# Kernel optimization log

Hardware: AMD Instinct MI355X
Metric: run time of the kernel (lower is better)

## Reference

```python
import jax, jax.numpy as jnp
import numpy as np

EMBED_DIM = 768
NUM_HEADS = 12
HEAD_DIM = EMBED_DIM // NUM_HEADS


def setup_inputs() -> dict:
    key = jax.random.key(0)
    ks = jax.random.split(key, 9)
    B, N, D = 8, 1024, EMBED_DIM
    s = 1.0 / np.sqrt(D)
    x = jax.random.normal(ks[0], (B, N, D), dtype=jnp.float32)
    Wq = jax.random.normal(ks[1], (D, D), dtype=jnp.float32) * s
    bq = jnp.zeros((D,), dtype=jnp.float32)
    Wk = jax.random.normal(ks[2], (D, D), dtype=jnp.float32) * s
    bk = jnp.zeros((D,), dtype=jnp.float32)
    Wv = jax.random.normal(ks[3], (D, D), dtype=jnp.float32) * s
    bv = jnp.zeros((D,), dtype=jnp.float32)
    Wo = jax.random.normal(ks[4], (D, D), dtype=jnp.float32) * s
    bo = jnp.zeros((D,), dtype=jnp.float32)
    return {"x": x, "Wq": Wq, "bq": bq, "Wk": Wk, "bk": bk,
            "Wv": Wv, "bv": bv, "Wo": Wo, "bo": bo}


def reference(x, Wq, bq, Wk, bk, Wv, bv, Wo, bo):
    B, N, D = x.shape
    H, Hd = NUM_HEADS, HEAD_DIM
    # torch Linear: y = x @ W.T + b
    q = (x @ Wq.T + bq).reshape(B, N, H, Hd).transpose(0, 2, 1, 3)  # [B,H,N,Hd]
    k = (x @ Wk.T + bk).reshape(B, N, H, Hd).transpose(0, 2, 1, 3)
    v = (x @ Wv.T + bv).reshape(B, N, H, Hd).transpose(0, 2, 1, 3)
    # NOTE: original scales by embed_dim**-0.5 (not head_dim)
    scale = jnp.asarray(D, x.dtype) ** -0.5
    scores = jnp.einsum('bhnd,bhmd->bhnm', q, k) * scale  # [B,H,N,N]
    attn = jax.nn.softmax(scores, axis=-1)
    out = jnp.einsum('bhnm,bhmd->bhnd', attn, v)  # dropout: identity in eval
    out = out.transpose(0, 2, 1, 3).reshape(B, N, D)
    return out @ Wo.T + bo
```

## Files before the change

kernel.cpp:

```cpp
#include <hip/hip_runtime.h>
#include <math.h>


typedef __bf16 bf16x8 __attribute__((ext_vector_type(8)));
typedef float  f32x4  __attribute__((ext_vector_type(4)));
typedef unsigned u32x2 __attribute__((ext_vector_type(2)));
typedef unsigned u32x4 __attribute__((ext_vector_type(4)));
typedef unsigned short ushort_t;

__device__ __forceinline__ unsigned short f2bf(float f) {
    unsigned u = __float_as_uint(f);
    u += 0x7fffu + ((u >> 16) & 1u);
    return (unsigned short)(u >> 16);
}

#define GLL16(g, l)                                                                        \
    __builtin_amdgcn_global_load_lds((const __attribute__((address_space(1))) void*)(g),   \
                                     (__attribute__((address_space(3))) void*)(l), 16, 0, 0)

__global__ __launch_bounds__(256)
void cast_all(const float* __restrict__ x,
              const float* __restrict__ w0, const float* __restrict__ w1,
              const float* __restrict__ w2, const float* __restrict__ w3,
              ushort_t* __restrict__ xb, ushort_t* __restrict__ wb0,
              ushort_t* __restrict__ wb1, ushort_t* __restrict__ wb2,
              ushort_t* __restrict__ wb3)
{
    const int y = blockIdx.y;
    const float* s; ushort_t* d; int n;
    switch (y) {
        case 0:  s = x;  d = xb;  n = 8192 * 768; break;
        case 1:  s = w0; d = wb0; n = 768 * 768;  break;
        case 2:  s = w1; d = wb1; n = 768 * 768;  break;
        case 3:  s = w2; d = wb2; n = 768 * 768;  break;
        default: s = w3; d = wb3; n = 768 * 768;  break;
    }
    const int i = (blockIdx.x * 256 + threadIdx.x) * 8;
    if (i >= n) return;
    const float4 f0 = *(const float4*)(s + i);
    const float4 f1 = *(const float4*)(s + i + 4);
    ushort4 p0, p1;
    p0.x = f2bf(f0.x); p0.y = f2bf(f0.y); p0.z = f2bf(f0.z); p0.w = f2bf(f0.w);
    p1.x = f2bf(f1.x); p1.y = f2bf(f1.y); p1.z = f2bf(f1.z); p1.w = f2bf(f1.w);
    *(ushort4*)(d + i)     = p0;
    *(ushort4*)(d + i + 4) = p1;
}

__device__ __forceinline__ void gemm_core_mfma(
    const ushort_t* __restrict__ A, const ushort_t* __restrict__ W,
    int m0, int n0, f32x4 acc[4][4])
{
    __shared__ ushort_t As[128 * 32];
    __shared__ ushort_t Ws[128 * 32];
    const int tid = threadIdx.x;
    const int L   = tid & 63;
    const int wv  = tid >> 6;
    const int wr  = wv >> 1, wc = wv & 1;
    const int c   = L & 15,  g  = L >> 4;

    const int c0 = tid, c1 = tid + 256;
    const ushort_t* a0 = A + (size_t)(m0 + (c0 >> 2)) * 768 + (c0 & 3) * 8;
    const ushort_t* a1 = A + (size_t)(m0 + (c1 >> 2)) * 768 + (c1 & 3) * 8;
    const ushort_t* w0 = W + (size_t)(n0 + (c0 >> 2)) * 768 + (c0 & 3) * 8;
    const ushort_t* w1 = W + (size_t)(n0 + (c1 >> 2)) * 768 + (c1 & 3) * 8;

#pragma unroll
    for (int i = 0; i < 4; ++i)
#pragma unroll
        for (int j = 0; j < 4; ++j) acc[i][j] = (f32x4){0.f, 0.f, 0.f, 0.f};

    for (int k0 = 0; k0 < 768; k0 += 32) {
        __syncthreads();
        GLL16(a0 + k0, &As[(size_t)c0 * 8]);
        GLL16(a1 + k0, &As[(size_t)c1 * 8]);
        GLL16(w0 + k0, &Ws[(size_t)c0 * 8]);
        GLL16(w1 + k0, &Ws[(size_t)c1 * 8]);
        __syncthreads();
        bf16x8 af[4], bfr[4];
#pragma unroll
        for (int i = 0; i < 4; ++i)
            af[i] = *(const bf16x8*)&As[(wr * 64 + i * 16 + c) * 32 + g * 8];
#pragma unroll
        for (int j = 0; j < 4; ++j)
            bfr[j] = *(const bf16x8*)&Ws[(wc * 64 + j * 16 + c) * 32 + g * 8];
#pragma unroll
        for (int i = 0; i < 4; ++i)
#pragma unroll
            for (int j = 0; j < 4; ++j)
                acc[i][j] = __builtin_amdgcn_mfma_f32_16x16x32_bf16(
                    af[i], bfr[j], acc[i][j], 0, 0, 0);
    }
}

__global__ __launch_bounds__(256, 2)
void gemm_qkv(const ushort_t* __restrict__ xb,
              const ushort_t* __restrict__ wqb, const ushort_t* __restrict__ wkb,
              const ushort_t* __restrict__ wvb,
              const float* __restrict__ bq, const float* __restrict__ bk,
              const float* __restrict__ bv,
              ushort_t* __restrict__ Qh, ushort_t* __restrict__ Kl,
              ushort_t* __restrict__ Vl)
{
    const int z = blockIdx.z;
    const ushort_t* W   = (z == 0) ? wqb : (z == 1) ? wkb : wvb;
    const float*    bia = (z == 0) ? bq  : (z == 1) ? bk  : bv;
    const int m0 = blockIdx.y * 128, n0 = blockIdx.x * 128;
    f32x4 acc[4][4];
    gemm_core_mfma(xb, W, m0, n0, acc);

    const int tid = threadIdx.x, L = tid & 63, wv2 = tid >> 6;
    const int wr = wv2 >> 1, wc = wv2 & 1, c = L & 15, g = L >> 4;
#pragma unroll
    for (int i = 0; i < 4; ++i) {
        const int row0 = m0 + wr * 64 + i * 16 + g * 4;
        const int b = row0 >> 10;
        const int n = row0 & 1023;
#pragma unroll
        for (int j = 0; j < 4; ++j) {
            const int col = n0 + wc * 64 + j * 16 + c;
            const int h = col >> 6, hd = col & 63;
            const int bh = b * 12 + h;
            const float bsv = bia[col];
            if (z == 0) {
                ushort_t* dst = Qh + ((size_t)bh * 1024 + n) * 64 + hd;
#pragma unroll
                for (int r = 0; r < 4; ++r)
                    dst[(size_t)r * 64] = f2bf(acc[i][j][r] + bsv);
            } else if (z == 1) {
                const int tau = n >> 4, cK = n & 15;
                const int u = hd >> 5, gK = (hd >> 3) & 3, j8 = hd & 7;
                ushort_t* dst = Kl + (((size_t)bh * 64 + tau) * 2 + u) * 512
                              + gK * 128 + cK * 8 + j8;
#pragma unroll
                for (int r = 0; r < 4; ++r)
                    dst[r * 8] = f2bf(acc[i][j][r] + bsv);
            } else {
                const int ht = hd >> 4, cV = hd & 15;
                const int T = n >> 6, u = (n >> 5) & 1, gV = (n >> 3) & 3, j0 = n & 7;
                ushort4 pk;
                pk.x = f2bf(acc[i][j][0] + bsv);
                pk.y = f2bf(acc[i][j][1] + bsv);
                pk.z = f2bf(acc[i][j][2] + bsv);
                pk.w = f2bf(acc[i][j][3] + bsv);
                *(ushort4*)&Vl[(((size_t)(bh * 4 + ht) * 16 + T) * 2 + u) * 512
                               + gV * 128 + cV * 8 + j0] = pk;
            }
        }
    }
}

__global__ __launch_bounds__(256, 2)
void gemm_outp(const ushort_t* __restrict__ attnb, const ushort_t* __restrict__ wob,
               const float* __restrict__ bo, float* __restrict__ out)
{
    const int m0 = blockIdx.y * 128, n0 = blockIdx.x * 128;
    f32x4 acc[4][4];
    gemm_core_mfma(attnb, wob, m0, n0, acc);
    const int tid = threadIdx.x, L = tid & 63, wv2 = tid >> 6;
    const int wr = wv2 >> 1, wc = wv2 & 1, c = L & 15, g = L >> 4;
#pragma unroll
    for (int i = 0; i < 4; ++i) {
        const int row = m0 + wr * 64 + i * 16 + g * 4;
#pragma unroll
        for (int j = 0; j < 4; ++j) {
            const int col = n0 + wc * 64 + j * 16 + c;
            const float bsv = bo[col];
#pragma unroll
            for (int r = 0; r < 4; ++r)
                out[(size_t)(row + r) * 768 + col] = acc[i][j][r] + bsv;
        }
    }
}

__global__ __launch_bounds__(64, 3)
void flash_bf16(const ushort_t* __restrict__ Q, const ushort_t* __restrict__ Kl,
                const ushort_t* __restrict__ Vl, ushort_t* __restrict__ attnb)
{
    __shared__ ushort_t Ps[2][16 * 68];
    const int L = threadIdx.x;
    const int c = L & 15, g = L >> 4;
    const int bh = blockIdx.y, q0 = blockIdx.x * 32;
    const float SC2 = 0.05205954985329743f;

    const ushort_t* Qp = Q + ((size_t)bh * 1024 + q0 + c) * 64 + g * 8;
    bf16x8 qf[2][2];
    qf[0][0] = *(const bf16x8*)Qp;
    qf[0][1] = *(const bf16x8*)(Qp + 32);
    qf[1][0] = *(const bf16x8*)(Qp + 16 * 64);
    qf[1][1] = *(const bf16x8*)(Qp + 16 * 64 + 32);

    const ushort_t* Kb = Kl + (size_t)bh * 65536 + (size_t)L * 8;
    const ushort_t* Vb = Vl + (size_t)bh * 65536 + (size_t)L * 8;

    f32x4 o[2][4];
#pragma unroll
    for (int w = 0; w < 2; ++w)
#pragma unroll
        for (int ht = 0; ht < 4; ++ht) o[w][ht] = (f32x4){0.f, 0.f, 0.f, 0.f};
    float ls[2] = {0.f, 0.f};

    bf16x8 kf0[4], kf1[4];
#pragma unroll
    for (int ct = 0; ct < 4; ++ct) {
        kf0[ct] = *(const bf16x8*)(Kb + (size_t)(ct * 2 + 0) * 512);
        kf1[ct] = *(const bf16x8*)(Kb + (size_t)(ct * 2 + 1) * 512);
    }

    for (int T = 0; T < 16; ++T) {
        bf16x8 vf0[4], vf1[4];
#pragma unroll
        for (int ht = 0; ht < 4; ++ht) {
            const ushort_t* vp = Vb + (size_t)((ht * 16 + T) * 2) * 512;
            vf0[ht] = *(const bf16x8*)vp;
            vf1[ht] = *(const bf16x8*)(vp + 512);
        }
        f32x4 s[2][4];
#pragma unroll
        for (int w = 0; w < 2; ++w)
#pragma unroll
            for (int ct = 0; ct < 4; ++ct) {
                f32x4 zz = (f32x4){0.f, 0.f, 0.f, 0.f};
                zz = __builtin_amdgcn_mfma_f32_16x16x32_bf16(kf0[ct], qf[w][0], zz, 0, 0, 0);
                zz = __builtin_amdgcn_mfma_f32_16x16x32_bf16(kf1[ct], qf[w][1], zz, 0, 0, 0);
                s[w][ct] = zz;
            }
        const int Tn = (T < 15) ? T + 1 : 15;
#pragma unroll
        for (int ct = 0; ct < 4; ++ct) {
            const ushort_t* kp = Kb + (size_t)((Tn * 4 + ct) * 2) * 512;
            kf0[ct] = *(const bf16x8*)kp;
            kf1[ct] = *(const bf16x8*)(kp + 512);
        }
#pragma unroll
        for (int w = 0; w < 2; ++w) {
            unsigned pw[4][2];
#pragma unroll
            for (int ct = 0; ct < 4; ++ct) {
                float p[4];
#pragma unroll
                for (int r = 0; r < 4; ++r) p[r] = exp2f(s[w][ct][r] * SC2);
                const unsigned w01 = __builtin_amdgcn_perm(
                    __float_as_uint(p[1]), __float_as_uint(p[0]), 0x07060302u);
                const unsigned w23 = __builtin_amdgcn_perm(
                    __float_as_uint(p[3]), __float_as_uint(p[2]), 0x07060302u);
                pw[ct][0] = w01;
                pw[ct][1] = w23;
                ls[w] += __uint_as_float(w01 << 16) + __uint_as_float(w01 & 0xffff0000u)
                       + __uint_as_float(w23 << 16) + __uint_as_float(w23 & 0xffff0000u);
            }
#pragma unroll
            for (int ct = 0; ct < 4; ++ct)
                *(u32x2*)&Ps[w][c * 68 + ct * 16 + g * 4] = (u32x2){pw[ct][0], pw[ct][1]};
        }
#pragma unroll
        for (int w = 0; w < 2; ++w) {
            const int pb = c * 68 + g * 8;
            const u32x4 pa  = *(const u32x4*)&Ps[w][pb];
            const u32x4 pbv = *(const u32x4*)&Ps[w][pb + 32];
            const bf16x8 pf0 = __builtin_bit_cast(bf16x8, pa);
            const bf16x8 pf1 = __builtin_bit_cast(bf16x8, pbv);
#pragma unroll
            for (int ht = 0; ht < 4; ++ht) {
                o[w][ht] = __builtin_amdgcn_mfma_f32_16x16x32_bf16(vf0[ht], pf0, o[w][ht], 0, 0, 0);
                o[w][ht] = __builtin_amdgcn_mfma_f32_16x16x32_bf16(vf1[ht], pf1, o[w][ht], 0, 0, 0);
            }
        }
    }

    const int b = bh / 12, h = bh % 12;
#pragma unroll
    for (int w = 0; w < 2; ++w) {
        float l = ls[w];
        l += __shfl_xor(l, 16);
        l += __shfl_xor(l, 32);
        const float inv = 1.f / l;
#pragma unroll
        for (int ht = 0; ht < 4; ++ht) {
            const unsigned w0 = (unsigned)f2bf(o[w][ht][0] * inv)
                              | ((unsigned)f2bf(o[w][ht][1] * inv) << 16);
            const unsigned w1 = (unsigned)f2bf(o[w][ht][2] * inv)
                              | ((unsigned)f2bf(o[w][ht][3] * inv) << 16);
            *(u32x2*)&Ps[w][c * 68 + ht * 16 + g * 4] = (u32x2){w0, w1};
        }
#pragma unroll
        for (int e = 0; e < 2; ++e) {
            const int row = e * 8 + (L >> 3);
            const int ch  = L & 7;
            const int si  = row * 68 + ch * 8;
            const u32x2 t0 = *(const u32x2*)&Ps[w][si];
            const u32x2 t1 = *(const u32x2*)&Ps[w][si + 4];
            *(u32x4*)&attnb[((size_t)(b * 1024 + q0 + w * 16 + row)) * 768 + h * 64 + ch * 8]
                = (u32x4){t0.x, t0.y, t1.x, t1.y};
        }
    }
}

extern "C" void kernel_launch(void* const* d_in, const int* in_sizes, int n_in,
                              void* d_out, int out_size, void* d_ws, size_t ws_size,
                              hipStream_t stream)
{
    const float* x  = (const float*)d_in[0];
    const float* Wq = (const float*)d_in[1];
    const float* bq = (const float*)d_in[2];
    const float* Wk = (const float*)d_in[3];
    const float* bk = (const float*)d_in[4];
    const float* Wv = (const float*)d_in[5];
    const float* bv = (const float*)d_in[6];
    const float* Wo = (const float*)d_in[7];
    const float* bo = (const float*)d_in[8];
    float* out = (float*)d_out;

    char* ws = (char*)d_ws;
    ushort_t* xb    = (ushort_t*)(ws);
    ushort_t* wqb   = (ushort_t*)(ws + 12582912);
    ushort_t* wkb   = (ushort_t*)(ws + 12582912 + 1179648);
    ushort_t* wvb   = (ushort_t*)(ws + 12582912 + 2359296);
    ushort_t* wob   = (ushort_t*)(ws + 12582912 + 3538944);
    ushort_t* Qh    = (ushort_t*)(ws + 17301504);
    ushort_t* Kl    = (ushort_t*)(ws + 29884416);
    ushort_t* Vl    = (ushort_t*)(ws + 42467328);
    ushort_t* attnb = (ushort_t*)(ws + 55050240);

    cast_all<<<dim3(3072, 5), 256, 0, stream>>>(x, Wq, Wk, Wv, Wo,
                                                xb, wqb, wkb, wvb, wob);
    gemm_qkv<<<dim3(6, 64, 3), 256, 0, stream>>>(xb, wqb, wkb, wvb,
                                                 bq, bk, bv, Qh, Kl, Vl);
    flash_bf16<<<dim3(32, 96), 64, 0, stream>>>(Qh, Kl, Vl, attnb);
    gemm_outp<<<dim3(6, 64), 256, 0, stream>>>(attnb, wob, bo, out);
}
```

Baseline: 212.9 us.

## Split flash KV loop across two waves and stage QKV epilogue stores through LDS

The flash attention kernel now runs two waves per block, each covering half of the key/value tiles. Their partial outputs and row sums are merged through shared memory, which is valid because the softmax uses no running max. The QKV GEMM epilogue now stages each 16-row tile in shared memory so Q, K and V are written with 16-byte vector stores instead of scattered 2-byte stores. This adds an LDS merge and barrier in exchange for more parallelism per query tile, and it drops the previous K prefetch pipelining.

```diff
diff --git a/kernel.cpp b/kernel.cpp
--- a/kernel.cpp
+++ b/kernel.cpp
@@ -12,6 +12,9 @@
     unsigned u = __float_as_uint(f);
     u += 0x7fffu + ((u >> 16) & 1u);
     return (unsigned short)(u >> 16);
+}
+__device__ __forceinline__ unsigned pk16(unsigned short lo, unsigned short hi) {
+    return (unsigned)lo | ((unsigned)hi << 16);
 }
 
 #define GLL16(g, l)                                                                        \
@@ -48,10 +51,10 @@
 
 __device__ __forceinline__ void gemm_core_mfma(
     const ushort_t* __restrict__ A, const ushort_t* __restrict__ W,
-    int m0, int n0, f32x4 acc[4][4])
-{
-    __shared__ ushort_t As[128 * 32];
-    __shared__ ushort_t Ws[128 * 32];
+    int m0, int n0, ushort_t* smem, f32x4 acc[4][4])
+{
+    ushort_t* As = smem;
+    ushort_t* Ws = smem + 4096;
     const int tid = threadIdx.x;
     const int L   = tid & 63;
     const int wv  = tid >> 6;
@@ -101,50 +104,70 @@
               ushort_t* __restrict__ Qh, ushort_t* __restrict__ Kl,
               ushort_t* __restrict__ Vl)
 {
+    __shared__ ushort_t smem[8192];
     const int z = blockIdx.z;
     const ushort_t* W   = (z == 0) ? wqb : (z == 1) ? wkb : wvb;
     const float*    bia = (z == 0) ? bq  : (z == 1) ? bk  : bv;
     const int m0 = blockIdx.y * 128, n0 = blockIdx.x * 128;
     f32x4 acc[4][4];
-    gemm_core_mfma(xb, W, m0, n0, acc);
+    gemm_core_mfma(xb, W, m0, n0, smem, acc);
 
     const int tid = threadIdx.x, L = tid & 63, wv2 = tid >> 6;
     const int wr = wv2 >> 1, wc = wv2 & 1, c = L & 15, g = L >> 4;
+    ushort_t* scr = smem + wv2 * 1280;
+    const int h = (n0 + wc * 64) >> 6;
+    float bsv[4];
+#pragma unroll
+    for (int j = 0; j < 4; ++j) bsv[j] = bia[n0 + wc * 64 + j * 16 + c];
+
+    __syncthreads();
 #pragma unroll
     for (int i = 0; i < 4; ++i) {
-        const int row0 = m0 + wr * 64 + i * 16 + g * 4;
-        const int b = row0 >> 10;
-        const int n = row0 & 1023;
-#pragma unroll
-        for (int j = 0; j < 4; ++j) {
-            const int col = n0 + wc * 64 + j * 16 + c;
-            const int h = col >> 6, hd = col & 63;
-            const int bh = b * 12 + h;
-            const float bsv = bia[col];
+        const int rowg = m0 + wr * 64 + i * 16;
+        const int b  = rowg >> 10;
+        const int nb = rowg & 1023;
+        const int bh = b * 12 + h;
+        if (z < 2) {
+#pragma unroll
+            for (int j = 0; j < 4; ++j)
+#pragma unroll
+                for (int r = 0; r < 4; ++r)
+                    scr[(g * 4 + r) * 72 + j * 16 + c] = f2bf(acc[i][j][r] + bsv[j]);
             if (z == 0) {
-                ushort_t* dst = Qh + ((size_t)bh * 1024 + n) * 64 + hd;
-#pragma unroll
-                for (int r = 0; r < 4; ++r)
-                    dst[(size_t)r * 64] = f2bf(acc[i][j][r] + bsv);
-            } else if (z == 1) {
-                const int tau = n >> 4, cK = n & 15;
-                const int u = hd >> 5, gK = (hd >> 3) & 3, j8 = hd & 7;
-                ushort_t* dst = Kl + (((size_t)bh * 64 + tau) * 2 + u) * 512
-                              + gK * 128 + cK * 8 + j8;
-#pragma unroll
-                for (int r = 0; r < 4; ++r)
-                    dst[r * 8] = f2bf(acc[i][j][r] + bsv);
+                const int row = L >> 2, qp = L & 3;
+                const u32x4 v0 = *(const u32x4*)&scr[row * 72 + qp * 16];
+                const u32x4 v1 = *(const u32x4*)&scr[row * 72 + qp * 16 + 8];
+                ushort_t* dst = Qh + ((size_t)bh * 1024 + nb + row) * 64 + qp * 16;
+                *(u32x4*)dst       = v0;
+                *(u32x4*)(dst + 8) = v1;
             } else {
-                const int ht = hd >> 4, cV = hd & 15;
-                const int T = n >> 6, u = (n >> 5) & 1, gV = (n >> 3) & 3, j0 = n & 7;
-                ushort4 pk;
-                pk.x = f2bf(acc[i][j][0] + bsv);
-                pk.y = f2bf(acc[i][j][1] + bsv);
-                pk.z = f2bf(acc[i][j][2] + bsv);
-                pk.w = f2bf(acc[i][j][3] + bsv);
-                *(ushort4*)&Vl[(((size_t)(bh * 4 + ht) * 16 + T) * 2 + u) * 512
-                               + gV * 128 + cV * 8 + j0] = pk;
-            }
+                const int n16 = L >> 2, q1 = L & 3;
+                const u32x4 va = *(const u32x4*)&scr[n16 * 72 + q1 * 8];
+                const u32x4 vb2 = *(const u32x4*)&scr[n16 * 72 + q1 * 8 + 32];
+                ushort_t* base = Kl + (size_t)bh * 65536 + (size_t)(nb >> 4) * 1024;
+                *(u32x4*)&base[q1 * 128 + n16 * 8]       = va;
+                *(u32x4*)&base[512 + q1 * 128 + n16 * 8] = vb2;
+            }
+        } else {
+#pragma unroll
+            for (int j = 0; j < 4; ++j) {
+                const unsigned w01 = pk16(f2bf(acc[i][j][0] + bsv[j]),
+                                          f2bf(acc[i][j][1] + bsv[j]));
+                const unsigned w23 = pk16(f2bf(acc[i][j][2] + bsv[j]),
+                                          f2bf(acc[i][j][3] + bsv[j]));
+                const int a = (j * 16 + c) * 20 + g * 4;
+                *(unsigned*)&scr[a]     = w01;
+                *(unsigned*)&scr[a + 2] = w23;
+            }
+            const u32x2 r0 = *(const u32x2*)&scr[L * 20];
+            const u32x2 r1 = *(const u32x2*)&scr[L * 20 + 4];
+            const u32x2 r2 = *(const u32x2*)&scr[L * 20 + 8];
+            const u32x2 r3 = *(const u32x2*)&scr[L * 20 + 12];
+            const int ht = L >> 4, cV = L & 15;
+            const int T = nb >> 6, u = (nb >> 5) & 1, gVa = (nb >> 3) & 3;
+            ushort_t* vb = Vl + (((size_t)(bh * 4 + ht) * 16 + T) * 2 + u) * 512 + cV * 8;
+            *(u32x4*)&vb[gVa * 128]       = (u32x4){r0.x, r0.y, r1.x, r1.y};
+            *(u32x4*)&vb[(gVa + 1) * 128] = (u32x4){r2.x, r2.y, r3.x, r3.y};
         }
     }
 }
@@ -153,9 +176,10 @@
 void gemm_outp(const ushort_t* __restrict__ attnb, const ushort_t* __restrict__ wob,
                const float* __restrict__ bo, float* __restrict__ out)
 {
+    __shared__ ushort_t smem[8192];
     const int m0 = blockIdx.y * 128, n0 = blockIdx.x * 128;
     f32x4 acc[4][4];
-    gemm_core_mfma(attnb, wob, m0, n0, acc);
+    gemm_core_mfma(attnb, wob, m0, n0, smem, acc);
     const int tid = threadIdx.x, L = tid & 63, wv2 = tid >> 6;
     const int wr = wv2 >> 1, wc = wv2 & 1, c = L & 15, g = L >> 4;
 #pragma unroll
@@ -164,21 +188,22 @@
 #pragma unroll
         for (int j = 0; j < 4; ++j) {
             const int col = n0 + wc * 64 + j * 16 + c;
-            const float bsv = bo[col];
+            const float bsvo = bo[col];
 #pragma unroll
             for (int r = 0; r < 4; ++r)
-                out[(size_t)(row + r) * 768 + col] = acc[i][j][r] + bsv;
-        }
-    }
-}
-
-__global__ __launch_bounds__(64, 3)
+                out[(size_t)(row + r) * 768 + col] = acc[i][j][r] + bsvo;
+        }
+    }
+}
+
+__global__ __launch_bounds__(128, 4)
 void flash_bf16(const ushort_t* __restrict__ Q, const ushort_t* __restrict__ Kl,
                 const ushort_t* __restrict__ Vl, ushort_t* __restrict__ attnb)
 {
-    __shared__ ushort_t Ps[2][16 * 68];
-    const int L = threadIdx.x;
-    const int c = L & 15, g = L >> 4;
+    __shared__ ushort_t Ps[2][2][16 * 68];
+    __shared__ f32x4 Comb[64 * 9];
+    const int tid = threadIdx.x;
+    const int wv = tid >> 6, L = tid & 63, c = L & 15, g = L >> 4;
     const int bh = blockIdx.y, q0 = blockIdx.x * 32;
     const float SC2 = 0.05205954985329743f;
 
@@ -186,8 +211,8 @@
     bf16x8 qf[2][2];
     qf[0][0] = *(const bf16x8*)Qp;
     qf[0][1] = *(const bf16x8*)(Qp + 32);
-    qf[1][0] = *(const bf16x8*)(Qp + 16 * 64);
-    qf[1][1] = *(const bf16x8*)(Qp + 16 * 64 + 32);
+    qf[1][0] = *(const bf16x8*)(Qp + 1024);
+    qf[1][1] = *(const bf16x8*)(Qp + 1056);
 
     const ushort_t* Kb = Kl + (size_t)bh * 65536 + (size_t)L * 8;
     const ushort_t* Vb = Vl + (size_t)bh * 65536 + (size_t)L * 8;
@@ -199,98 +224,99 @@
         for (int ht = 0; ht < 4; ++ht) o[w][ht] = (f32x4){0.f, 0.f, 0.f, 0.f};
     float ls[2] = {0.f, 0.f};
 
-    bf16x8 kf0[4], kf1[4];
-#pragma unroll
-    for (int ct = 0; ct < 4; ++ct) {
-        kf0[ct] = *(const bf16x8*)(Kb + (size_t)(ct * 2 + 0) * 512);
-        kf1[ct] = *(const bf16x8*)(Kb + (size_t)(ct * 2 + 1) * 512);
-    }
-
-    for (int T = 0; T < 16; ++T) {
-        bf16x8 vf0[4], vf1[4];
-#pragma unroll
-        for (int ht = 0; ht < 4; ++ht) {
-            const ushort_t* vp = Vb + (size_t)((ht * 16 + T) * 2) * 512;
-            vf0[ht] = *(const bf16x8*)vp;
-            vf1[ht] = *(const bf16x8*)(vp + 512);
-        }
-        f32x4 s[2][4];
-#pragma unroll
-        for (int w = 0; w < 2; ++w)
+    const int Tbeg = wv * 8;
+    for (int T = Tbeg; T < Tbeg + 8; ++T) {
+        bf16x8 kf0[4], kf1[4];
+#pragma unroll
+        for (int ct = 0; ct < 4; ++ct) {
+            const ushort_t* kp = Kb + (size_t)((T * 4 + ct) * 2) * 512;
+            kf0[ct] = *(const bf16x8*)kp;
+            kf1[ct] = *(const bf16x8*)(kp + 512);
+        }
+#pragma unroll
+        for (int w = 0; w < 2; ++w) {
+            f32x4 s[4];
 #pragma unroll
             for (int ct = 0; ct < 4; ++ct) {
                 f32x4 zz = (f32x4){0.f, 0.f, 0.f, 0.f};
                 zz = __builtin_amdgcn_mfma_f32_16x16x32_bf16(kf0[ct], qf[w][0], zz, 0, 0, 0);
                 zz = __builtin_amdgcn_mfma_f32_16x16x32_bf16(kf1[ct], qf[w][1], zz, 0, 0, 0);
-                s[w][ct] = zz;
-            }
-        const int Tn = (T < 15) ? T + 1 : 15;
-#pragma unroll
-        for (int ct = 0; ct < 4; ++ct) {
-            const ushort_t* kp = Kb + (size_t)((Tn * 4 + ct) * 2) * 512;
-            kf0[ct] = *(const bf16x8*)kp;
-            kf1[ct] = *(const bf16x8*)(kp + 512);
-        }
-#pragma unroll
-        for (int w = 0; w < 2; ++w) {
-            unsigned pw[4][2];
+                s[ct] = zz;
+            }
 #pragma unroll
             for (int ct = 0; ct < 4; ++ct) {
                 float p[4];
 #pragma unroll
-                for (int r = 0; r < 4; ++r) p[r] = exp2f(s[w][ct][r] * SC2);
+                for (int r = 0; r < 4; ++r) p[r] = exp2f(s[ct][r] * SC2);
                 const unsigned w01 = __builtin_amdgcn_perm(
                     __float_as_uint(p[1]), __float_as_uint(p[0]), 0x07060302u);
                 const unsigned w23 = __builtin_amdgcn_perm(
                     __float_as_uint(p[3]), __float_as_uint(p[2]), 0x07060302u);
-                pw[ct][0] = w01;
-                pw[ct][1] = w23;
                 ls[w] += __uint_as_float(w01 << 16) + __uint_as_float(w01 & 0xffff0000u)
                        + __uint_as_float(w23 << 16) + __uint_as_float(w23 & 0xffff0000u);
-            }
-#pragma unroll
-            for (int ct = 0; ct < 4; ++ct)
-                *(u32x2*)&Ps[w][c * 68 + ct * 16 + g * 4] = (u32x2){pw[ct][0], pw[ct][1]};
-        }
+                *(u32x2*)&Ps[wv][w][c * 68 + ct * 16 + g * 4] = (u32x2){w01, w23};
+            }
+        }
+        const int pb = c * 68 + g * 8;
+        bf16x8 pf[2][2];
 #pragma unroll
         for (int w = 0; w < 2; ++w) {
-            const int pb = c * 68 + g * 8;
-            const u32x4 pa  = *(const u32x4*)&Ps[w][pb];
-            const u32x4 pbv = *(const u32x4*)&Ps[w][pb + 32];
-            const bf16x8 pf0 = __builtin_bit_cast(bf16x8, pa);
-            const bf16x8 pf1 = __builtin_bit_cast(bf16x8, pbv);
+            pf[w][0] = __builtin_bit_cast(bf16x8, *(const u32x4*)&Ps[wv][w][pb]);
+            pf[w][1] = __builtin_bit_cast(bf16x8, *(const u32x4*)&Ps[wv][w][pb + 32]);
+        }
+#pragma unroll
+        for (int ht = 0; ht < 4; ++ht) {
+            const ushort_t* vp = Vb + (size_t)((ht * 16 + T) * 2) * 512;
+            const bf16x8 v0 = *(const bf16x8*)vp;
+            const bf16x8 v1 = *(const bf16x8*)(vp + 512);
+#pragma unroll
+            for (int w = 0; w < 2; ++w) {
+                o[w][ht] = __builtin_amdgcn_mfma_f32_16x16x32_bf16(v0, pf[w][0], o[w][ht], 0, 0, 0);
+                o[w][ht] = __builtin_amdgcn_mfma_f32_16x16x32_bf16(v1, pf[w][1], o[w][ht], 0, 0, 0);
+            }
+        }
+    }
+
+    if (wv == 1) {
+#pragma unroll
+        for (int w = 0; w < 2; ++w)
+#pragma unroll
+            for (int ht = 0; ht < 4; ++ht) Comb[L * 9 + w * 4 + ht] = o[w][ht];
+        Comb[L * 9 + 8] = (f32x4){ls[0], ls[1], 0.f, 0.f};
+    }
+    __syncthreads();
+    if (wv == 0) {
+#pragma unroll
+        for (int w = 0; w < 2; ++w)
+#pragma unroll
+            for (int ht = 0; ht < 4; ++ht) o[w][ht] += Comb[L * 9 + w * 4 + ht];
+        const f32x4 lw = Comb[L * 9 + 8];
+        ls[0] += lw.x;
+        ls[1] += lw.y;
+
+        const int b = bh / 12, h = bh % 12;
+#pragma unroll
+        for (int w = 0; w < 2; ++w) {
+            float l = ls[w];
+            l += __shfl_xor(l, 16);
+            l += __shfl_xor(l, 32);
+            const float inv = 1.f / l;
 #pragma unroll
             for (int ht = 0; ht < 4; ++ht) {
-                o[w][ht] = __builtin_amdgcn_mfma_f32_16x16x32_bf16(vf0[ht], pf0, o[w][ht], 0, 0, 0);
-                o[w][ht] = __builtin_amdgcn_mfma_f32_16x16x32_bf16(vf1[ht], pf1, o[w][ht], 0, 0, 0);
-            }
-        }
-    }
-
-    const int b = bh / 12, h = bh % 12;
-#pragma unroll
-    for (int w = 0; w < 2; ++w) {
-        float l = ls[w];
-        l += __shfl_xor(l, 16);
-        l += __shfl_xor(l, 32);
-        const float inv = 1.f / l;
-#pragma unroll
-        for (int ht = 0; ht < 4; ++ht) {
-            const unsigned w0 = (unsigned)f2bf(o[w][ht][0] * inv)
-                              | ((unsigned)f2bf(o[w][ht][1] * inv) << 16);
-            const unsigned w1 = (unsigned)f2bf(o[w][ht][2] * inv)
-                              | ((unsigned)f2bf(o[w][ht][3] * inv) << 16);
-            *(u32x2*)&Ps[w][c * 68 + ht * 16 + g * 4] = (u32x2){w0, w1};
-        }
-#pragma unroll
-        for (int e = 0; e < 2; ++e) {
-            const int row = e * 8 + (L >> 3);
-            const int ch  = L & 7;
-            const int si  = row * 68 + ch * 8;
-            const u32x2 t0 = *(const u32x2*)&Ps[w][si];
-            const u32x2 t1 = *(const u32x2*)&Ps[w][si + 4];
-            *(u32x4*)&attnb[((size_t)(b * 1024 + q0 + w * 16 + row)) * 768 + h * 64 + ch * 8]
-                = (u32x4){t0.x, t0.y, t1.x, t1.y};
+                const unsigned w0 = pk16(f2bf(o[w][ht][0] * inv), f2bf(o[w][ht][1] * inv));
+                const unsigned w1 = pk16(f2bf(o[w][ht][2] * inv), f2bf(o[w][ht][3] * inv));
+                *(u32x2*)&Ps[0][w][c * 68 + ht * 16 + g * 4] = (u32x2){w0, w1};
+            }
+#pragma unroll
+            for (int e = 0; e < 2; ++e) {
+                const int row = e * 8 + (L >> 3);
+                const int ch  = L & 7;
+                const int si  = row * 68 + ch * 8;
+                const u32x2 t0 = *(const u32x2*)&Ps[0][w][si];
+                const u32x2 t1 = *(const u32x2*)&Ps[0][w][si + 4];
+                *(u32x4*)&attnb[((size_t)(b * 1024 + q0 + w * 16 + row)) * 768 + h * 64 + ch * 8]
+                    = (u32x4){t0.x, t0.y, t1.x, t1.y};
+            }
         }
     }
 }
@@ -325,6 +351,6 @@
                                                 xb, wqb, wkb, wvb, wob);
     gemm_qkv<<<dim3(6, 64, 3), 256, 0, stream>>>(xb, wqb, wkb, wvb,
                                                  bq, bk, bv, Qh, Kl, Vl);
-    flash_bf16<<<dim3(32, 96), 64, 0, stream>>>(Qh, Kl, Vl, attnb);
+    flash_bf16<<<dim3(32, 96), 128, 0, stream>>>(Qh, Kl, Vl, attnb);
     gemm_outp<<<dim3(6, 64), 256, 0, stream>>>(attnb, wob, bo, out);
 }
```

After: 219.1 us. +2.9%, slower.
